# Kernel optimization log

Hardware: AMD Instinct MI355X
Metric: run time of the kernel (lower is better)

## Reference

```python
import jax, jax.numpy as jnp
import numpy as np

# CUBA LIF neuron params (from DECOLLENetwork.__init__)
THRESH = 1.25
CUR_DECAY = 0.25
VOLT_DECAY = 0.03
TAU_GRAD = 0.03
SCALE_GRAD = 3.0
SPIKE_PROB = 0.1  # input spike density


@jax.custom_vjp
def spike_fn(v):
    # Heaviside threshold with surrogate gradient (lava-dl slayer Spike)
    return (v >= THRESH).astype(v.dtype)

def _spike_fwd(v):
    return spike_fn(v), v

def _spike_bwd(v, g):
    # surrogate: scale_rho / tau_rho * exp(-|v - theta| / tau_rho)
    sg = (SCALE_GRAD / TAU_GRAD) * jnp.exp(-jnp.abs(v - THRESH) / TAU_GRAD)
    return (g * sg,)

spike_fn.defvjp(_spike_fwd, _spike_bwd)


def cuba_voltage(z):
    """Leaky-integrator recurrence over the trailing time axis.
    z: [B, N, T] synaptic current input. Returns pre-reset voltage [B, N, T].
    current[t] = (1-cd)*current[t-1] + z[t]
    voltage[t] = (1-vd)*voltage[t-1] + current[t]; hard reset to 0 on spike.
    """
    B, N, _ = z.shape
    def step(carry, zt):
        cur, volt = carry
        cur = (1.0 - CUR_DECAY) * cur + zt
        volt = (1.0 - VOLT_DECAY) * volt + cur
        volt_next = jnp.where(volt >= THRESH, 0.0, volt)  # Loihi-style hard reset
        return (cur, volt_next), volt
    init = (jnp.zeros((B, N), z.dtype), jnp.zeros((B, N), z.dtype))
    _, volts = jax.lax.scan(step, init, jnp.moveaxis(z, -1, 0))  # [T, B, N]
    return jnp.moveaxis(volts, 0, -1)  # [B, N, T]


def setup_inputs() -> dict:
    key = jax.random.key(0)
    k_x, k1, k2, k3, k4 = jax.random.split(key, 5)
    B, F_IN, T = 32, 512, 256
    H, OUT = 1024, 128
    spike = (jax.random.uniform(k_x, (B, F_IN, T)) < SPIKE_PROB).astype(jnp.float32)
    W1 = jax.random.normal(k1, (H, F_IN), jnp.float32) / np.sqrt(F_IN)
    W2 = jax.random.normal(k2, (H, H), jnp.float32) / np.sqrt(H)
    R1 = jax.random.normal(k3, (OUT, H), jnp.float32) / np.sqrt(H)
    R2 = jax.random.normal(k4, (OUT, H), jnp.float32) / np.sqrt(H)
    return {"spike": spike, "W1": W1, "W2": W2, "R1": R1, "R2": R2}


def reference(spike, W1, W2, R1, R2):
    spikes, readouts, voltages, counts = [], [], [], []
    x = spike
    for W in (W1, W2):
        # synapse: dense GEMM per timestep (input detached, DECOLLE local learning)
        z = jnp.einsum('hf,bft->bht', W, jax.lax.stop_gradient(x))
        v = cuba_voltage(z)
        s = spike_fn(v)
        voltages.append(v)
        spikes.append(s)
        counts.append(jnp.mean(jax.lax.stop_gradient(s)))
        x = s
    for R, s in zip((R1, R2), spikes):
        # readout: one batched GEMM over all timesteps (same math as per-t Linear)
        readouts.append(jnp.einsum('oh,bht->bot', R, s))
    return (tuple(spikes), tuple(readouts), tuple(voltages), tuple(counts))
```

## Files before the change

kernel.cpp:

```cpp
#include <hip/hip_runtime.h>
#include <hip/hip_bf16.h>


#define S_SZ 8388608
#define R_SZ 1048576

typedef __attribute__((ext_vector_type(8))) short v8s;
typedef __attribute__((ext_vector_type(4))) float v4f;
typedef __attribute__((ext_vector_type(8))) unsigned short u8us;

static __device__ __forceinline__ unsigned short f2bf(float x) {
  union { __hip_bfloat16 b; unsigned short u; } cv;
  cv.b = __float2bfloat16(x);
  return cv.u;
}
static __device__ __forceinline__ float bf2f(unsigned short u) {
  union { __hip_bfloat16 b; unsigned short u; } cv;
  cv.u = u;
  return __bfloat162float(cv.b);
}


__global__ __launch_bounds__(256) void split_all_kernel(
    const float* __restrict__ W1, const float* __restrict__ W2,
    const float* __restrict__ R1, const float* __restrict__ R2,
    unsigned short* __restrict__ w1s, unsigned short* __restrict__ w2s,
    unsigned short* __restrict__ r1s, unsigned short* __restrict__ r2s,
    int* __restrict__ cnt) {
  if (blockIdx.y == 0 && blockIdx.x == 0 && threadIdx.x == 0) {
    cnt[0] = 0; cnt[1] = 0;
  }
  const int i = blockIdx.x * 256 + threadIdx.x;
  const float* W; unsigned short* out; int N;
  switch (blockIdx.y) {
    case 0: W = W1; out = w1s; N = 524288; break;
    case 1: W = W2; out = w2s; N = 1048576; break;
    case 2: W = R1; out = r1s; N = 131072; break;
    default: W = R2; out = r2s; N = 131072; break;
  }
  if (i >= N) return;
  const float w0 = W[i];
  const unsigned short h = f2bf(w0);
  const float hf = bf2f(h);
  const float rm = w0 - hf;
  const unsigned short m = f2bf(rm);
  const float mf = bf2f(m);
  const unsigned short l = f2bf(rm - mf);
  out[i] = h; out[N + i] = m; out[2 * N + i] = l;
}

__global__ __launch_bounds__(256) void tcvt_kernel(const float* __restrict__ in,
                                                   unsigned short* __restrict__ out,
                                                   int R) {
  __shared__ float Ls[64][68];
  const int r0 = blockIdx.x * 64, c0 = blockIdx.y * 64, b = blockIdx.z;
  const int tid = threadIdx.x;
  const float* ip = in + ((size_t)b * R + r0) * 256 + c0;
#pragma unroll
  for (int it = 0; it < 4; ++it) {
    const int row = it * 16 + (tid >> 4), col = (tid & 15) * 4;
    const float4 v = *(const float4*)&ip[(size_t)row * 256 + col];
    *(float4*)&Ls[row][col] = v;
  }
  __syncthreads();
  const int c = tid >> 2, rs = (tid & 3) * 16;
  unsigned short h[16];
#pragma unroll
  for (int j = 0; j < 16; ++j) h[j] = f2bf(Ls[rs + j][c]);
  u8us p0, p1;
#pragma unroll
  for (int j = 0; j < 8; ++j) { p0[j] = h[j]; p1[j] = h[8 + j]; }
  unsigned short* op = out + ((size_t)b * 256 + c0 + c) * R + r0 + rs;
  *(u8us*)(op) = p0;
  *(u8us*)(op + 8) = p1;
}

__global__ __launch_bounds__(256) void gemm_mfma(
    const unsigned short* __restrict__ Asp,
    const unsigned short* __restrict__ XT,
    float* __restrict__ Z,
    int M, int K) {
  __shared__ unsigned short Alds[3 * 128 * 64];
  const int t0 = blockIdx.x * 64;
  const int m0 = blockIdx.y * 128;
  const int bg = blockIdx.z;
  const int tid = threadIdx.x;
  const int w = tid >> 6, lane = tid & 63;
  const int r = lane & 15, q = lane >> 4;
  const int wm = w >> 1, wt = w & 1;
  const int srow = lane >> 3, sslot = lane & 7;

  v4f acc[2][4][2];
#pragma unroll
  for (int ib = 0; ib < 2; ++ib)
#pragma unroll
    for (int f = 0; f < 4; ++f)
#pragma unroll
      for (int g = 0; g < 2; ++g) acc[ib][f][g] = (v4f){0.f, 0.f, 0.f, 0.f};

  const size_t MK = (size_t)M * K;
  const int nkc = K >> 6;

  for (int kc = 0; kc < nkc; ++kc) {
    const int k0 = kc << 6;
#pragma unroll
    for (int s = 0; s < 3; ++s)
#pragma unroll
      for (int c = 0; c < 4; ++c) {
        const int row = w * 32 + c * 8 + srow;
        const unsigned short* src = Asp + (size_t)s * MK + (size_t)(m0 + row) * K +
                                    k0 + ((sslot ^ (row & 7)) << 3);
        unsigned short* dst = &Alds[s * 8192 + (w * 32 + c * 8) * 64];
        __builtin_amdgcn_global_load_lds(
            (const __attribute__((address_space(1))) unsigned int*)src,
            (__attribute__((address_space(3))) unsigned int*)dst, 16, 0, 0);
      }
    v8s bfr[2][2][2];
#pragma unroll
    for (int ib = 0; ib < 2; ++ib) {
      const size_t xbase = ((size_t)(bg * 2 + ib) * 256) * K;
#pragma unroll
      for (int ks = 0; ks < 2; ++ks)
#pragma unroll
        for (int g = 0; g < 2; ++g) {
          const int t = t0 + wt * 32 + g * 16 + r;
          bfr[ib][ks][g] =
              *(const v8s*)(XT + xbase + (size_t)t * K + k0 + ks * 32 + q * 8);
        }
    }
    __syncthreads();
#pragma unroll
    for (int ks = 0; ks < 2; ++ks)
#pragma unroll
      for (int s = 0; s < 3; ++s)
#pragma unroll
        for (int f = 0; f < 4; ++f) {
          const int arow = wm * 64 + f * 16 + r;
          const v8s a = *(const v8s*)&Alds[s * 8192 + arow * 64 +
                                           (((ks * 4 + q) ^ (arow & 7)) << 3)];
#pragma unroll
          for (int ib = 0; ib < 2; ++ib) {
            acc[ib][f][0] = __builtin_amdgcn_mfma_f32_16x16x32_bf16(
                a, bfr[ib][ks][0], acc[ib][f][0], 0, 0, 0);
            acc[ib][f][1] = __builtin_amdgcn_mfma_f32_16x16x32_bf16(
                a, bfr[ib][ks][1], acc[ib][f][1], 0, 0, 0);
          }
        }
    __syncthreads();
  }
#pragma unroll
  for (int ib = 0; ib < 2; ++ib) {
    float* Zb = Z + ((size_t)(bg * 2 + ib) * M) * 256;
#pragma unroll
    for (int f = 0; f < 4; ++f)
#pragma unroll
      for (int g = 0; g < 2; ++g)
#pragma unroll
        for (int e = 0; e < 4; ++e)
          Zb[(size_t)(m0 + wm * 64 + f * 16 + q * 4 + e) * 256 +
             t0 + wt * 32 + g * 16 + r] = acc[ib][f][g][e];
  }
}

__global__ __launch_bounds__(256) void readout_mfma(
    const unsigned short* __restrict__ r1s, const unsigned short* __restrict__ r2s,
    const unsigned short* __restrict__ s1T, const unsigned short* __restrict__ s2T,
    float* __restrict__ O1, float* __restrict__ O2,
    const int* __restrict__ cnt, float* __restrict__ cc) {
  if (blockIdx.x == 0 && blockIdx.y == 0 && blockIdx.z == 0 && threadIdx.x == 0) {
    cc[0] = (float)cnt[0] * (1.0f / 8388608.0f);
    cc[1] = (float)cnt[1] * (1.0f / 8388608.0f);
  }
  const int K = 1024;
  const int t0 = blockIdx.x * 64;
  const int net = blockIdx.y;
  const int b = blockIdx.z;
  const unsigned short* __restrict__ Asp = net ? r2s : r1s;
  const unsigned short* __restrict__ XT =
      (net ? s2T : s1T) + (size_t)b * 256 * K;
  float* __restrict__ Zb = (net ? O2 : O1) + (size_t)b * 128 * 256;

  __shared__ unsigned short Alds[3 * 128 * 64];
  const int tid = threadIdx.x;
  const int w = tid >> 6, lane = tid & 63;
  const int r = lane & 15, q = lane >> 4;
  const int wm = w >> 1, wt = w & 1;
  const int srow = lane >> 3, sslot = lane & 7;

  v4f acc[4][2];
#pragma unroll
  for (int f = 0; f < 4; ++f)
#pragma unroll
    for (int g = 0; g < 2; ++g) acc[f][g] = (v4f){0.f, 0.f, 0.f, 0.f};

  const size_t MK = (size_t)128 * K;

  for (int kc = 0; kc < 16; ++kc) {
    const int k0 = kc << 6;
#pragma unroll
    for (int s = 0; s < 3; ++s)
#pragma unroll
      for (int c = 0; c < 4; ++c) {
        const int row = w * 32 + c * 8 + srow;
        const unsigned short* src = Asp + (size_t)s * MK + (size_t)row * K +
                                    k0 + ((sslot ^ (row & 7)) << 3);
        unsigned short* dst = &Alds[s * 8192 + (w * 32 + c * 8) * 64];
        __builtin_amdgcn_global_load_lds(
            (const __attribute__((address_space(1))) unsigned int*)src,
            (__attribute__((address_space(3))) unsigned int*)dst, 16, 0, 0);
      }
    v8s bfr[2][2];
#pragma unroll
    for (int ks = 0; ks < 2; ++ks)
#pragma unroll
      for (int g = 0; g < 2; ++g) {
        const int t = t0 + wt * 32 + g * 16 + r;
        bfr[ks][g] = *(const v8s*)(XT + (size_t)t * K + k0 + ks * 32 + q * 8);
      }
    __syncthreads();
#pragma unroll
    for (int ks = 0; ks < 2; ++ks)
#pragma unroll
      for (int s = 0; s < 3; ++s)
#pragma unroll
        for (int f = 0; f < 4; ++f) {
          const int arow = wm * 64 + f * 16 + r;
          const v8s a = *(const v8s*)&Alds[s * 8192 + arow * 64 +
                                           (((ks * 4 + q) ^ (arow & 7)) << 3)];
          acc[f][0] = __builtin_amdgcn_mfma_f32_16x16x32_bf16(
              a, bfr[ks][0], acc[f][0], 0, 0, 0);
          acc[f][1] = __builtin_amdgcn_mfma_f32_16x16x32_bf16(
              a, bfr[ks][1], acc[f][1], 0, 0, 0);
        }
    __syncthreads();
  }
#pragma unroll
  for (int f = 0; f < 4; ++f)
#pragma unroll
    for (int g = 0; g < 2; ++g)
#pragma unroll
      for (int e = 0; e < 4; ++e)
        Zb[(size_t)(wm * 64 + f * 16 + q * 4 + e) * 256 +
           t0 + wt * 32 + g * 16 + r] = acc[f][g][e];
}

__global__ __launch_bounds__(64) void scan_kernel(float* __restrict__ VZ,
                                                  float* __restrict__ S,
                                                  unsigned short* __restrict__ ST,
                                                  int* __restrict__ cnt) {
  const int g = blockIdx.x * 64 + threadIdx.x;
  float* vz = VZ + (size_t)g * 256;
  float* sp = S + (size_t)g * 256;
  unsigned short* st =
      ST ? ST + ((size_t)(g >> 10) * 256) * 1024 + (g & 1023) : nullptr;
  const float CD = 0.75f;
  const float VD = (float)(1.0 - 0.03);

  float4 buf[4][4];
#pragma unroll
  for (int i = 0; i < 4; ++i)
#pragma unroll
    for (int qq = 0; qq < 4; ++qq)
      buf[i][qq] = *(const float4*)(vz + i * 16 + qq * 4);

  float cur = 0.f, volt = 0.f;
  int c = 0;
#pragma unroll
  for (int tc = 0; tc < 16; ++tc) {
    float zv[16];
    *(float4*)&zv[0]  = buf[tc & 3][0];
    *(float4*)&zv[4]  = buf[tc & 3][1];
    *(float4*)&zv[8]  = buf[tc & 3][2];
    *(float4*)&zv[12] = buf[tc & 3][3];
    if (tc < 12) {
#pragma unroll
      for (int qq = 0; qq < 4; ++qq)
        buf[tc & 3][qq] = *(const float4*)(vz + (tc + 4) * 16 + qq * 4);
    }
    float vv[16], sv[16];
    unsigned short sb[16];
#pragma unroll
    for (int j = 0; j < 16; ++j) {
      cur = CD * cur + zv[j];
      volt = VD * volt + cur;
      vv[j] = volt;
      const bool spk = volt >= 1.25f;
      sv[j] = spk ? 1.0f : 0.0f;
      sb[j] = spk ? 0x3F80 : 0;
      c += spk ? 1 : 0;
      volt = spk ? 0.f : volt;
    }
    float4 o;
    o = {vv[0], vv[1], vv[2], vv[3]};     *(float4*)(vz + tc * 16 + 0) = o;
    o = {vv[4], vv[5], vv[6], vv[7]};     *(float4*)(vz + tc * 16 + 4) = o;
    o = {vv[8], vv[9], vv[10], vv[11]};   *(float4*)(vz + tc * 16 + 8) = o;
    o = {vv[12], vv[13], vv[14], vv[15]}; *(float4*)(vz + tc * 16 + 12) = o;
    o = {sv[0], sv[1], sv[2], sv[3]};     *(float4*)(sp + tc * 16 + 0) = o;
    o = {sv[4], sv[5], sv[6], sv[7]};     *(float4*)(sp + tc * 16 + 4) = o;
    o = {sv[8], sv[9], sv[10], sv[11]};   *(float4*)(sp + tc * 16 + 8) = o;
    o = {sv[12], sv[13], sv[14], sv[15]}; *(float4*)(sp + tc * 16 + 12) = o;
    if (st) {
#pragma unroll
      for (int j = 0; j < 16; ++j)
        st[(size_t)(tc * 16 + j) * 1024] = sb[j];
    }
  }
#pragma unroll
  for (int off = 32; off > 0; off >>= 1) c += __shfl_down(c, off);
  if (threadIdx.x == 0) atomicAdd(cnt, c);
}

__global__ void finalize_kernel(const int* __restrict__ cnt, float* __restrict__ c) {
  if (threadIdx.x == 0) {
    c[0] = (float)cnt[0] * (1.0f / 8388608.0f);
    c[1] = (float)cnt[1] * (1.0f / 8388608.0f);
  }
}


__global__ __launch_bounds__(256) void zero_r_kernel(float* __restrict__ r,
                                                     int* __restrict__ cnt) {
  int i = blockIdx.x * 256 + threadIdx.x;
  float4 z{0.f, 0.f, 0.f, 0.f};
  *(float4*)&r[(size_t)i * 4] = z;
  if (i == 0) { cnt[0] = 0; cnt[1] = 0; }
}

__global__ __launch_bounds__(256) void gemm_f32(
    const float* __restrict__ W, const float* __restrict__ X,
    float* __restrict__ Z, int M, int K) {
  const int T = 256;
  const int tt0 = blockIdx.x * 64;
  const int m0 = blockIdx.y * 128;
  const int b = blockIdx.z;
  const float* __restrict__ Xb = X + (size_t)b * K * T;
  float* __restrict__ Zb = Z + (size_t)b * M * T;
  __shared__ float Ws[16][132];
  __shared__ float Xs[16][68];
  const int tid = threadIdx.x;
  const int tx = tid & 15, ty = tid >> 4;
  const int ah = tid >> 1, ac = (tid & 1) * 8;
  const int bf = tid >> 4, btq = (tid & 15) * 4;
  float acc[8][4];
#pragma unroll
  for (int i = 0; i < 8; ++i)
#pragma unroll
    for (int j = 0; j < 4; ++j) acc[i][j] = 0.f;
  const float* wp = &W[(size_t)(m0 + ah) * K + ac];
  const float* xp = &Xb[(size_t)bf * T + tt0 + btq];
  for (int k0 = 0; k0 < K; k0 += 16) {
    float4 wa0 = *(const float4*)(wp + k0);
    float4 wa1 = *(const float4*)(wp + k0 + 4);
    float4 xv = *(const float4*)(xp + (size_t)k0 * T);
    __syncthreads();
    Ws[ac + 0][ah] = wa0.x; Ws[ac + 1][ah] = wa0.y;
    Ws[ac + 2][ah] = wa0.z; Ws[ac + 3][ah] = wa0.w;
    Ws[ac + 4][ah] = wa1.x; Ws[ac + 5][ah] = wa1.y;
    Ws[ac + 6][ah] = wa1.z; Ws[ac + 7][ah] = wa1.w;
    *(float4*)&Xs[bf][btq] = xv;
    __syncthreads();
#pragma unroll
    for (int f = 0; f < 16; ++f) {
      float4 a0 = *(const float4*)&Ws[f][ty * 8];
      float4 a1 = *(const float4*)&Ws[f][ty * 8 + 4];
      float4 xr = *(const float4*)&Xs[f][tx * 4];
      float av[8] = {a0.x, a0.y, a0.z, a0.w, a1.x, a1.y, a1.z, a1.w};
      float xw[4] = {xr.x, xr.y, xr.z, xr.w};
#pragma unroll
      for (int i = 0; i < 8; ++i)
#pragma unroll
        for (int j = 0; j < 4; ++j) acc[i][j] = fmaf(av[i], xw[j], acc[i][j]);
    }
  }
#pragma unroll
  for (int i = 0; i < 8; ++i) {
    float4 o{acc[i][0], acc[i][1], acc[i][2], acc[i][3]};
    *(float4*)&Zb[(size_t)(m0 + ty * 8 + i) * T + tt0 + tx * 4] = o;
  }
}

__global__ __launch_bounds__(256) void readout_kernel(
    const float* __restrict__ R1, const float* __restrict__ R2,
    const float* __restrict__ S1, const float* __restrict__ S2,
    float* __restrict__ O1, float* __restrict__ O2) {
  const int T = 256, K = 1024;
  const int tt0 = blockIdx.x * 64;
  const int kbeg = blockIdx.y * 256;
  const int zz = blockIdx.z;
  const int b = zz & 31;
  const float* __restrict__ R = (zz < 32) ? R1 : R2;
  const float* __restrict__ Sb = ((zz < 32) ? S1 : S2) + (size_t)b * K * T;
  float* __restrict__ Ob = ((zz < 32) ? O1 : O2) + (size_t)b * 128 * T;
  __shared__ float Ws[16][132];
  __shared__ float Xs[16][68];
  const int tid = threadIdx.x;
  const int tx = tid & 15, ty = tid >> 4;
  const int ah = tid >> 1, ac = (tid & 1) * 8;
  const int bf = tid >> 4, btq = (tid & 15) * 4;
  float acc[8][4];
#pragma unroll
  for (int i = 0; i < 8; ++i)
#pragma unroll
    for (int j = 0; j < 4; ++j) acc[i][j] = 0.f;
  const float* wp = &R[(size_t)ah * K + ac];
  const float* xp = &Sb[(size_t)bf * T + tt0 + btq];
  for (int k0 = kbeg; k0 < kbeg + 256; k0 += 16) {
    float4 wa0 = *(const float4*)(wp + k0);
    float4 wa1 = *(const float4*)(wp + k0 + 4);
    float4 xv = *(const float4*)(xp + (size_t)k0 * T);
    __syncthreads();
    Ws[ac + 0][ah] = wa0.x; Ws[ac + 1][ah] = wa0.y;
    Ws[ac + 2][ah] = wa0.z; Ws[ac + 3][ah] = wa0.w;
    Ws[ac + 4][ah] = wa1.x; Ws[ac + 5][ah] = wa1.y;
    Ws[ac + 6][ah] = wa1.z; Ws[ac + 7][ah] = wa1.w;
    *(float4*)&Xs[bf][btq] = xv;
    __syncthreads();
#pragma unroll
    for (int f = 0; f < 16; ++f) {
      float4 a0 = *(const float4*)&Ws[f][ty * 8];
      float4 a1 = *(const float4*)&Ws[f][ty * 8 + 4];
      float4 xr = *(const float4*)&Xs[f][tx * 4];
      float av[8] = {a0.x, a0.y, a0.z, a0.w, a1.x, a1.y, a1.z, a1.w};
      float xw[4] = {xr.x, xr.y, xr.z, xr.w};
#pragma unroll
      for (int i = 0; i < 8; ++i)
#pragma unroll
        for (int j = 0; j < 4; ++j) acc[i][j] = fmaf(av[i], xw[j], acc[i][j]);
    }
  }
#pragma unroll
  for (int i = 0; i < 8; ++i)
#pragma unroll
    for (int j = 0; j < 4; ++j)
      atomicAdd(&Ob[(size_t)(ty * 8 + i) * T + tt0 + tx * 4 + j], acc[i][j]);
}

extern "C" void kernel_launch(void* const* d_in, const int* in_sizes, int n_in,
                              void* d_out, int out_size, void* d_ws, size_t ws_size,
                              hipStream_t stream) {
  const float* spike = (const float*)d_in[0];
  const float* W1 = (const float*)d_in[1];
  const float* W2 = (const float*)d_in[2];
  const float* R1 = (const float*)d_in[3];
  const float* R2 = (const float*)d_in[4];

  float* out = (float*)d_out;
  float* s1 = out;
  float* s2 = out + S_SZ;
  float* r1 = out + 2 * S_SZ;
  float* r2 = out + 2 * S_SZ + R_SZ;
  float* v1 = out + 2 * S_SZ + 2 * R_SZ;
  float* v2 = out + 2 * S_SZ + 2 * R_SZ + S_SZ;
  float* cc = out + 4 * S_SZ + 2 * R_SZ;

  int* cnt = (int*)d_ws;
  unsigned short* w1s = (unsigned short*)((char*)d_ws + 64);
  unsigned short* w2s = w1s + 3 * 524288;
  unsigned short* r1s = w2s + 3 * 1048576;
  unsigned short* r2s = r1s + 3 * 131072;
  unsigned short* xT  = r2s + 3 * 131072;
  unsigned short* s1T = xT + 4194304;
  unsigned short* s2T = s1T + 8388608;
  const size_t WS_NEED = 53000000;

  if (ws_size >= WS_NEED) {
    split_all_kernel<<<dim3(4096, 4), 256, 0, stream>>>(W1, W2, R1, R2, w1s, w2s,
                                                        r1s, r2s, cnt);
    tcvt_kernel<<<dim3(8, 4, 32), 256, 0, stream>>>(spike, xT, 512);
    gemm_mfma<<<dim3(4, 8, 16), 256, 0, stream>>>(w1s, xT, v1, 1024, 512);
    scan_kernel<<<512, 64, 0, stream>>>(v1, s1, s1T, cnt + 0);
    gemm_mfma<<<dim3(4, 8, 16), 256, 0, stream>>>(w2s, s1T, v2, 1024, 1024);
    scan_kernel<<<512, 64, 0, stream>>>(v2, s2, s2T, cnt + 1);
    readout_mfma<<<dim3(4, 2, 32), 256, 0, stream>>>(r1s, r2s, s1T, s2T, r1, r2,
                                                     cnt, cc);
  } else {
    zero_r_kernel<<<2048, 256, 0, stream>>>(r1, cnt);
    gemm_f32<<<dim3(4, 8, 32), 256, 0, stream>>>(W1, spike, v1, 1024, 512);
    scan_kernel<<<512, 64, 0, stream>>>(v1, s1, nullptr, cnt + 0);
    gemm_f32<<<dim3(4, 8, 32), 256, 0, stream>>>(W2, s1, v2, 1024, 1024);
    scan_kernel<<<512, 64, 0, stream>>>(v2, s2, nullptr, cnt + 1);
    readout_kernel<<<dim3(4, 4, 64), 256, 0, stream>>>(R1, R2, s1, s2, r1, r2);
    finalize_kernel<<<1, 1, 0, stream>>>(cnt, cc);
  }
}
```

Baseline: 347.9 us.

## Double-buffer split-A LDS tiles to overlap global loads with MFMA compute

Both the layer GEMM and readout GEMM now keep two LDS buffers, each holding one bf16 split slice of the A tile. The next slice is prefetched while MFMAs run on the current one, and B fragments are loaded ahead in alternating register sets. Previously all three slices were loaded, then a barrier, then compute, with no overlap. The cost is three times as many barriers per K-chunk and extra registers for two B fragment sets, which may lower occupancy.

```diff
diff --git a/kernel.cpp b/kernel.cpp
--- a/kernel.cpp
+++ b/kernel.cpp
@@ -80,7 +80,7 @@
     const unsigned short* __restrict__ XT,
     float* __restrict__ Z,
     int M, int K) {
-  __shared__ unsigned short Alds[3 * 128 * 64];
+  __shared__ unsigned short Alds[2][128 * 64];
   const int t0 = blockIdx.x * 64;
   const int m0 = blockIdx.y * 128;
   const int bg = blockIdx.z;
@@ -89,33 +89,32 @@
   const int r = lane & 15, q = lane >> 4;
   const int wm = w >> 1, wt = w & 1;
   const int srow = lane >> 3, sslot = lane & 7;
-
-  v4f acc[2][4][2];
-#pragma unroll
-  for (int ib = 0; ib < 2; ++ib)
-#pragma unroll
-    for (int f = 0; f < 4; ++f)
-#pragma unroll
-      for (int g = 0; g < 2; ++g) acc[ib][f][g] = (v4f){0.f, 0.f, 0.f, 0.f};
-
   const size_t MK = (size_t)M * K;
   const int nkc = K >> 6;
 
-  for (int kc = 0; kc < nkc; ++kc) {
+  v4f acc[2][4][2];
+#pragma unroll
+  for (int ib = 0; ib < 2; ++ib)
+#pragma unroll
+    for (int f = 0; f < 4; ++f)
+#pragma unroll
+      for (int g = 0; g < 2; ++g) acc[ib][f][g] = (v4f){0.f, 0.f, 0.f, 0.f};
+
+  auto STAGE = [&](int buf, int s, int kc) {
     const int k0 = kc << 6;
 #pragma unroll
-    for (int s = 0; s < 3; ++s)
-#pragma unroll
-      for (int c = 0; c < 4; ++c) {
-        const int row = w * 32 + c * 8 + srow;
-        const unsigned short* src = Asp + (size_t)s * MK + (size_t)(m0 + row) * K +
-                                    k0 + ((sslot ^ (row & 7)) << 3);
-        unsigned short* dst = &Alds[s * 8192 + (w * 32 + c * 8) * 64];
-        __builtin_amdgcn_global_load_lds(
-            (const __attribute__((address_space(1))) unsigned int*)src,
-            (__attribute__((address_space(3))) unsigned int*)dst, 16, 0, 0);
-      }
-    v8s bfr[2][2][2];
+    for (int c = 0; c < 4; ++c) {
+      const int row = w * 32 + c * 8 + srow;
+      const unsigned short* src = Asp + (size_t)s * MK + (size_t)(m0 + row) * K +
+                                  k0 + ((sslot ^ (row & 7)) << 3);
+      unsigned short* dst = &Alds[buf][(w * 32 + c * 8) * 64];
+      __builtin_amdgcn_global_load_lds(
+          (const __attribute__((address_space(1))) unsigned int*)src,
+          (__attribute__((address_space(3))) unsigned int*)dst, 16, 0, 0);
+    }
+  };
+  auto BLOAD = [&](v8s (&bfr)[2][2][2], int kc) {
+    const int k0 = kc << 6;
 #pragma unroll
     for (int ib = 0; ib < 2; ++ib) {
       const size_t xbase = ((size_t)(bg * 2 + ib) * 256) * K;
@@ -128,26 +127,41 @@
               *(const v8s*)(XT + xbase + (size_t)t * K + k0 + ks * 32 + q * 8);
         }
     }
-    __syncthreads();
+  };
+  auto COMPUTE = [&](int buf, v8s (&bfr)[2][2][2]) {
 #pragma unroll
     for (int ks = 0; ks < 2; ++ks)
 #pragma unroll
-      for (int s = 0; s < 3; ++s)
-#pragma unroll
-        for (int f = 0; f < 4; ++f) {
-          const int arow = wm * 64 + f * 16 + r;
-          const v8s a = *(const v8s*)&Alds[s * 8192 + arow * 64 +
+      for (int f = 0; f < 4; ++f) {
+        const int arow = wm * 64 + f * 16 + r;
+        const v8s a = *(const v8s*)&Alds[buf][arow * 64 +
                                            (((ks * 4 + q) ^ (arow & 7)) << 3)];
 #pragma unroll
-          for (int ib = 0; ib < 2; ++ib) {
-            acc[ib][f][0] = __builtin_amdgcn_mfma_f32_16x16x32_bf16(
-                a, bfr[ib][ks][0], acc[ib][f][0], 0, 0, 0);
-            acc[ib][f][1] = __builtin_amdgcn_mfma_f32_16x16x32_bf16(
-                a, bfr[ib][ks][1], acc[ib][f][1], 0, 0, 0);
-          }
+        for (int ib = 0; ib < 2; ++ib) {
+          acc[ib][f][0] = __builtin_amdgcn_mfma_f32_16x16x32_bf16(
+              a, bfr[ib][ks][0], acc[ib][f][0], 0, 0, 0);
+          acc[ib][f][1] = __builtin_amdgcn_mfma_f32_16x16x32_bf16(
+              a, bfr[ib][ks][1], acc[ib][f][1], 0, 0, 0);
         }
-    __syncthreads();
-  }
+      }
+  };
+
+  v8s bA[2][2][2], bB[2][2][2];
+  STAGE(0, 0, 0);
+  BLOAD(bA, 0);
+  __syncthreads();
+  int buf = 0;
+  for (int kc = 0; kc < nkc; kc += 2) {
+    STAGE(buf ^ 1, 1, kc);     COMPUTE(buf, bA); __syncthreads(); buf ^= 1;
+    STAGE(buf ^ 1, 2, kc);     COMPUTE(buf, bA); __syncthreads(); buf ^= 1;
+    STAGE(buf ^ 1, 0, kc + 1); BLOAD(bB, kc + 1);
+                               COMPUTE(buf, bA); __syncthreads(); buf ^= 1;
+    STAGE(buf ^ 1, 1, kc + 1); COMPUTE(buf, bB); __syncthreads(); buf ^= 1;
+    STAGE(buf ^ 1, 2, kc + 1); COMPUTE(buf, bB); __syncthreads(); buf ^= 1;
+    if (kc + 2 < nkc) { STAGE(buf ^ 1, 0, kc + 2); BLOAD(bA, kc + 2); }
+                               COMPUTE(buf, bB); __syncthreads(); buf ^= 1;
+  }
+
 #pragma unroll
   for (int ib = 0; ib < 2; ++ib) {
     float* Zb = Z + ((size_t)(bg * 2 + ib) * M) * 256;
@@ -176,16 +190,17 @@
   const int net = blockIdx.y;
   const int b = blockIdx.z;
   const unsigned short* __restrict__ Asp = net ? r2s : r1s;
-  const unsigned short* __restrict__ XT =
-      (net ? s2T : s1T) + (size_t)b * 256 * K;
+  const unsigned short* __restrict__ XT = (net ? s2T : s1T) + (size_t)b * 256 * K;
   float* __restrict__ Zb = (net ? O2 : O1) + (size_t)b * 128 * 256;
 
-  __shared__ unsigned short Alds[3 * 128 * 64];
+  __shared__ unsigned short Alds[2][128 * 64];
   const int tid = threadIdx.x;
   const int w = tid >> 6, lane = tid & 63;
   const int r = lane & 15, q = lane >> 4;
   const int wm = w >> 1, wt = w & 1;
   const int srow = lane >> 3, sslot = lane & 7;
+  const size_t MK = (size_t)128 * K;
+  const int nkc = 16;
 
   v4f acc[4][2];
 #pragma unroll
@@ -193,23 +208,21 @@
 #pragma unroll
     for (int g = 0; g < 2; ++g) acc[f][g] = (v4f){0.f, 0.f, 0.f, 0.f};
 
-  const size_t MK = (size_t)128 * K;
-
-  for (int kc = 0; kc < 16; ++kc) {
+  auto STAGE = [&](int buf, int s, int kc) {
     const int k0 = kc << 6;
 #pragma unroll
-    for (int s = 0; s < 3; ++s)
-#pragma unroll
-      for (int c = 0; c < 4; ++c) {
-        const int row = w * 32 + c * 8 + srow;
-        const unsigned short* src = Asp + (size_t)s * MK + (size_t)row * K +
-                                    k0 + ((sslot ^ (row & 7)) << 3);
-        unsigned short* dst = &Alds[s * 8192 + (w * 32 + c * 8) * 64];
-        __builtin_amdgcn_global_load_lds(
-            (const __attribute__((address_space(1))) unsigned int*)src,
-            (__attribute__((address_space(3))) unsigned int*)dst, 16, 0, 0);
-      }
-    v8s bfr[2][2];
+    for (int c = 0; c < 4; ++c) {
+      const int row = w * 32 + c * 8 + srow;
+      const unsigned short* src = Asp + (size_t)s * MK + (size_t)row * K +
+                                  k0 + ((sslot ^ (row & 7)) << 3);
+      unsigned short* dst = &Alds[buf][(w * 32 + c * 8) * 64];
+      __builtin_amdgcn_global_load_lds(
+          (const __attribute__((address_space(1))) unsigned int*)src,
+          (__attribute__((address_space(3))) unsigned int*)dst, 16, 0, 0);
+    }
+  };
+  auto BLOAD = [&](v8s (&bfr)[2][2], int kc) {
+    const int k0 = kc << 6;
 #pragma unroll
     for (int ks = 0; ks < 2; ++ks)
 #pragma unroll
@@ -217,23 +230,38 @@
         const int t = t0 + wt * 32 + g * 16 + r;
         bfr[ks][g] = *(const v8s*)(XT + (size_t)t * K + k0 + ks * 32 + q * 8);
       }
-    __syncthreads();
+  };
+  auto COMPUTE = [&](int buf, v8s (&bfr)[2][2]) {
 #pragma unroll
     for (int ks = 0; ks < 2; ++ks)
 #pragma unroll
-      for (int s = 0; s < 3; ++s)
-#pragma unroll
-        for (int f = 0; f < 4; ++f) {
-          const int arow = wm * 64 + f * 16 + r;
-          const v8s a = *(const v8s*)&Alds[s * 8192 + arow * 64 +
+      for (int f = 0; f < 4; ++f) {
+        const int arow = wm * 64 + f * 16 + r;
+        const v8s a = *(const v8s*)&Alds[buf][arow * 64 +
                                            (((ks * 4 + q) ^ (arow & 7)) << 3)];
-          acc[f][0] = __builtin_amdgcn_mfma_f32_16x16x32_bf16(
-              a, bfr[ks][0], acc[f][0], 0, 0, 0);
-          acc[f][1] = __builtin_amdgcn_mfma_f32_16x16x32_bf16(
-              a, bfr[ks][1], acc[f][1], 0, 0, 0);
-        }
-    __syncthreads();
-  }
+        acc[f][0] = __builtin_amdgcn_mfma_f32_16x16x32_bf16(
+            a, bfr[ks][0], acc[f][0], 0, 0, 0);
+        acc[f][1] = __builtin_amdgcn_mfma_f32_16x16x32_bf16(
+            a, bfr[ks][1], acc[f][1], 0, 0, 0);
+      }
+  };
+
+  v8s bA[2][2], bB[2][2];
+  STAGE(0, 0, 0);
+  BLOAD(bA, 0);
+  __syncthreads();
+  int buf = 0;
+  for (int kc = 0; kc < nkc; kc += 2) {
+    STAGE(buf ^ 1, 1, kc);     COMPUTE(buf, bA); __syncthreads(); buf ^= 1;
+    STAGE(buf ^ 1, 2, kc);     COMPUTE(buf, bA); __syncthreads(); buf ^= 1;
+    STAGE(buf ^ 1, 0, kc + 1); BLOAD(bB, kc + 1);
+                               COMPUTE(buf, bA); __syncthreads(); buf ^= 1;
+    STAGE(buf ^ 1, 1, kc + 1); COMPUTE(buf, bB); __syncthreads(); buf ^= 1;
+    STAGE(buf ^ 1, 2, kc + 1); COMPUTE(buf, bB); __syncthreads(); buf ^= 1;
+    if (kc + 2 < nkc) { STAGE(buf ^ 1, 0, kc + 2); BLOAD(bA, kc + 2); }
+                               COMPUTE(buf, bB); __syncthreads(); buf ^= 1;
+  }
+
 #pragma unroll
   for (int f = 0; f < 4; ++f)
 #pragma unroll
```

Result: no change. 346.1 us (-0.5%).

## Use two-term bf16 weight split and load GEMM operands directly to registers

Applied to the files above, without the earlier changes.

Weights are now split into two bf16 terms instead of three, which cuts MFMA work and weight traffic by a third. The GEMM and readout kernels no longer stage A tiles through LDS with global_load_lds and barriers. Each wave instead loads its A and B fragments straight from global memory into registers. This removes the synchronisation and LDS traffic, but A rows are now reloaded per wave without sharing, and the two-term split lowers weight precision, which may matter near the spike threshold.

```diff
diff --git a/kernel.cpp b/kernel.cpp
--- a/kernel.cpp
+++ b/kernel.cpp
@@ -42,11 +42,8 @@
   const float w0 = W[i];
   const unsigned short h = f2bf(w0);
   const float hf = bf2f(h);
-  const float rm = w0 - hf;
-  const unsigned short m = f2bf(rm);
-  const float mf = bf2f(m);
-  const unsigned short l = f2bf(rm - mf);
-  out[i] = h; out[N + i] = m; out[2 * N + i] = l;
+  const unsigned short m = f2bf(w0 - hf);
+  out[i] = h; out[N + i] = m;
 }
 
 __global__ __launch_bounds__(256) void tcvt_kernel(const float* __restrict__ in,
@@ -75,12 +72,11 @@
   *(u8us*)(op + 8) = p1;
 }
 
-__global__ __launch_bounds__(256) void gemm_mfma(
+__global__ __launch_bounds__(256) void gemm_mfma_reg(
     const unsigned short* __restrict__ Asp,
     const unsigned short* __restrict__ XT,
     float* __restrict__ Z,
     int M, int K) {
-  __shared__ unsigned short Alds[3 * 128 * 64];
   const int t0 = blockIdx.x * 64;
   const int m0 = blockIdx.y * 128;
   const int bg = blockIdx.z;
@@ -88,66 +84,57 @@
   const int w = tid >> 6, lane = tid & 63;
   const int r = lane & 15, q = lane >> 4;
   const int wm = w >> 1, wt = w & 1;
-  const int srow = lane >> 3, sslot = lane & 7;
-
-  v4f acc[2][4][2];
-#pragma unroll
-  for (int ib = 0; ib < 2; ++ib)
-#pragma unroll
-    for (int f = 0; f < 4; ++f)
-#pragma unroll
-      for (int g = 0; g < 2; ++g) acc[ib][f][g] = (v4f){0.f, 0.f, 0.f, 0.f};
-
   const size_t MK = (size_t)M * K;
   const int nkc = K >> 6;
 
+  v4f acc[2][4][2];
+#pragma unroll
+  for (int ib = 0; ib < 2; ++ib)
+#pragma unroll
+    for (int f = 0; f < 4; ++f)
+#pragma unroll
+      for (int g = 0; g < 2; ++g) acc[ib][f][g] = (v4f){0.f, 0.f, 0.f, 0.f};
+
+  const unsigned short* aB = Asp + (size_t)(m0 + wm * 64 + r) * K + q * 8;
+  const unsigned short* bB0 =
+      XT + ((size_t)(bg * 2 + 0) * 256 + t0 + wt * 32 + r) * K + q * 8;
+  const unsigned short* bB1 =
+      XT + ((size_t)(bg * 2 + 1) * 256 + t0 + wt * 32 + r) * K + q * 8;
+
   for (int kc = 0; kc < nkc; ++kc) {
     const int k0 = kc << 6;
-#pragma unroll
-    for (int s = 0; s < 3; ++s)
-#pragma unroll
-      for (int c = 0; c < 4; ++c) {
-        const int row = w * 32 + c * 8 + srow;
-        const unsigned short* src = Asp + (size_t)s * MK + (size_t)(m0 + row) * K +
-                                    k0 + ((sslot ^ (row & 7)) << 3);
-        unsigned short* dst = &Alds[s * 8192 + (w * 32 + c * 8) * 64];
-        __builtin_amdgcn_global_load_lds(
-            (const __attribute__((address_space(1))) unsigned int*)src,
-            (__attribute__((address_space(3))) unsigned int*)dst, 16, 0, 0);
+    v8s b[2][2][2];
+#pragma unroll
+    for (int ks = 0; ks < 2; ++ks)
+#pragma unroll
+      for (int g = 0; g < 2; ++g) {
+        b[0][ks][g] = *(const v8s*)(bB0 + (size_t)(g * 16) * K + k0 + ks * 32);
+        b[1][ks][g] = *(const v8s*)(bB1 + (size_t)(g * 16) * K + k0 + ks * 32);
       }
-    v8s bfr[2][2][2];
-#pragma unroll
-    for (int ib = 0; ib < 2; ++ib) {
-      const size_t xbase = ((size_t)(bg * 2 + ib) * 256) * K;
+    v8s a[2][4][2];
+#pragma unroll
+    for (int s = 0; s < 2; ++s)
+#pragma unroll
+      for (int f = 0; f < 4; ++f)
+#pragma unroll
+        for (int ks = 0; ks < 2; ++ks)
+          a[s][f][ks] =
+              *(const v8s*)(aB + s * MK + (size_t)(f * 16) * K + k0 + ks * 32);
+#pragma unroll
+    for (int s = 0; s < 2; ++s)
 #pragma unroll
       for (int ks = 0; ks < 2; ++ks)
 #pragma unroll
-        for (int g = 0; g < 2; ++g) {
-          const int t = t0 + wt * 32 + g * 16 + r;
-          bfr[ib][ks][g] =
-              *(const v8s*)(XT + xbase + (size_t)t * K + k0 + ks * 32 + q * 8);
-        }
-    }
-    __syncthreads();
-#pragma unroll
-    for (int ks = 0; ks < 2; ++ks)
-#pragma unroll
-      for (int s = 0; s < 3; ++s)
-#pragma unroll
-        for (int f = 0; f < 4; ++f) {
-          const int arow = wm * 64 + f * 16 + r;
-          const v8s a = *(const v8s*)&Alds[s * 8192 + arow * 64 +
-                                           (((ks * 4 + q) ^ (arow & 7)) << 3)];
+        for (int f = 0; f < 4; ++f)
 #pragma unroll
           for (int ib = 0; ib < 2; ++ib) {
             acc[ib][f][0] = __builtin_amdgcn_mfma_f32_16x16x32_bf16(
-                a, bfr[ib][ks][0], acc[ib][f][0], 0, 0, 0);
+                a[s][f][ks], b[ib][ks][0], acc[ib][f][0], 0, 0, 0);
             acc[ib][f][1] = __builtin_amdgcn_mfma_f32_16x16x32_bf16(
-                a, bfr[ib][ks][1], acc[ib][f][1], 0, 0, 0);
+                a[s][f][ks], b[ib][ks][1], acc[ib][f][1], 0, 0, 0);
           }
-        }
-    __syncthreads();
-  }
+  }
+
 #pragma unroll
   for (int ib = 0; ib < 2; ++ib) {
     float* Zb = Z + ((size_t)(bg * 2 + ib) * M) * 256;
@@ -162,7 +149,7 @@
   }
 }
 
-__global__ __launch_bounds__(256) void readout_mfma(
+__global__ __launch_bounds__(256) void readout_mfma_reg(
     const unsigned short* __restrict__ r1s, const unsigned short* __restrict__ r2s,
     const unsigned short* __restrict__ s1T, const unsigned short* __restrict__ s2T,
     float* __restrict__ O1, float* __restrict__ O2,
@@ -176,16 +163,14 @@
   const int net = blockIdx.y;
   const int b = blockIdx.z;
   const unsigned short* __restrict__ Asp = net ? r2s : r1s;
-  const unsigned short* __restrict__ XT =
-      (net ? s2T : s1T) + (size_t)b * 256 * K;
+  const unsigned short* __restrict__ XT = (net ? s2T : s1T) + (size_t)b * 256 * K;
   float* __restrict__ Zb = (net ? O2 : O1) + (size_t)b * 128 * 256;
 
-  __shared__ unsigned short Alds[3 * 128 * 64];
   const int tid = threadIdx.x;
   const int w = tid >> 6, lane = tid & 63;
   const int r = lane & 15, q = lane >> 4;
   const int wm = w >> 1, wt = w & 1;
-  const int srow = lane >> 3, sslot = lane & 7;
+  const size_t MK = (size_t)128 * K;
 
   v4f acc[4][2];
 #pragma unroll
@@ -193,47 +178,39 @@
 #pragma unroll
     for (int g = 0; g < 2; ++g) acc[f][g] = (v4f){0.f, 0.f, 0.f, 0.f};
 
-  const size_t MK = (size_t)128 * K;
+  const unsigned short* aB = Asp + (size_t)(wm * 64 + r) * K + q * 8;
+  const unsigned short* bB = XT + (size_t)(t0 + wt * 32 + r) * K + q * 8;
 
   for (int kc = 0; kc < 16; ++kc) {
     const int k0 = kc << 6;
-#pragma unroll
-    for (int s = 0; s < 3; ++s)
-#pragma unroll
-      for (int c = 0; c < 4; ++c) {
-        const int row = w * 32 + c * 8 + srow;
-        const unsigned short* src = Asp + (size_t)s * MK + (size_t)row * K +
-                                    k0 + ((sslot ^ (row & 7)) << 3);
-        unsigned short* dst = &Alds[s * 8192 + (w * 32 + c * 8) * 64];
-        __builtin_amdgcn_global_load_lds(
-            (const __attribute__((address_space(1))) unsigned int*)src,
-            (__attribute__((address_space(3))) unsigned int*)dst, 16, 0, 0);
-      }
-    v8s bfr[2][2];
+    v8s b[2][2];
 #pragma unroll
     for (int ks = 0; ks < 2; ++ks)
 #pragma unroll
-      for (int g = 0; g < 2; ++g) {
-        const int t = t0 + wt * 32 + g * 16 + r;
-        bfr[ks][g] = *(const v8s*)(XT + (size_t)t * K + k0 + ks * 32 + q * 8);
-      }
-    __syncthreads();
-#pragma unroll
-    for (int ks = 0; ks < 2; ++ks)
-#pragma unroll
-      for (int s = 0; s < 3; ++s)
+      for (int g = 0; g < 2; ++g)
+        b[ks][g] = *(const v8s*)(bB + (size_t)(g * 16) * K + k0 + ks * 32);
+    v8s a[2][4][2];
+#pragma unroll
+    for (int s = 0; s < 2; ++s)
+#pragma unroll
+      for (int f = 0; f < 4; ++f)
+#pragma unroll
+        for (int ks = 0; ks < 2; ++ks)
+          a[s][f][ks] =
+              *(const v8s*)(aB + s * MK + (size_t)(f * 16) * K + k0 + ks * 32);
+#pragma unroll
+    for (int s = 0; s < 2; ++s)
+#pragma unroll
+      for (int ks = 0; ks < 2; ++ks)
 #pragma unroll
         for (int f = 0; f < 4; ++f) {
-          const int arow = wm * 64 + f * 16 + r;
-          const v8s a = *(const v8s*)&Alds[s * 8192 + arow * 64 +
-                                           (((ks * 4 + q) ^ (arow & 7)) << 3)];
           acc[f][0] = __builtin_amdgcn_mfma_f32_16x16x32_bf16(
-              a, bfr[ks][0], acc[f][0], 0, 0, 0);
+              a[s][f][ks], b[ks][0], acc[f][0], 0, 0, 0);
           acc[f][1] = __builtin_amdgcn_mfma_f32_16x16x32_bf16(
-              a, bfr[ks][1], acc[f][1], 0, 0, 0);
+              a[s][f][ks], b[ks][1], acc[f][1], 0, 0, 0);
         }
-    __syncthreads();
-  }
+  }
+
 #pragma unroll
   for (int f = 0; f < 4; ++f)
 #pragma unroll
@@ -455,24 +432,24 @@
 
   int* cnt = (int*)d_ws;
   unsigned short* w1s = (unsigned short*)((char*)d_ws + 64);
-  unsigned short* w2s = w1s + 3 * 524288;
-  unsigned short* r1s = w2s + 3 * 1048576;
-  unsigned short* r2s = r1s + 3 * 131072;
-  unsigned short* xT  = r2s + 3 * 131072;
+  unsigned short* w2s = w1s + 2 * 524288;
+  unsigned short* r1s = w2s + 2 * 1048576;
+  unsigned short* r2s = r1s + 2 * 131072;
+  unsigned short* xT  = r2s + 2 * 131072;
   unsigned short* s1T = xT + 4194304;
   unsigned short* s2T = s1T + 8388608;
-  const size_t WS_NEED = 53000000;
+  const size_t WS_NEED = 48000000;
 
   if (ws_size >= WS_NEED) {
     split_all_kernel<<<dim3(4096, 4), 256, 0, stream>>>(W1, W2, R1, R2, w1s, w2s,
                                                         r1s, r2s, cnt);
     tcvt_kernel<<<dim3(8, 4, 32), 256, 0, stream>>>(spike, xT, 512);
-    gemm_mfma<<<dim3(4, 8, 16), 256, 0, stream>>>(w1s, xT, v1, 1024, 512);
+    gemm_mfma_reg<<<dim3(4, 8, 16), 256, 0, stream>>>(w1s, xT, v1, 1024, 512);
     scan_kernel<<<512, 64, 0, stream>>>(v1, s1, s1T, cnt + 0);
-    gemm_mfma<<<dim3(4, 8, 16), 256, 0, stream>>>(w2s, s1T, v2, 1024, 1024);
+    gemm_mfma_reg<<<dim3(4, 8, 16), 256, 0, stream>>>(w2s, s1T, v2, 1024, 1024);
     scan_kernel<<<512, 64, 0, stream>>>(v2, s2, s2T, cnt + 1);
-    readout_mfma<<<dim3(4, 2, 32), 256, 0, stream>>>(r1s, r2s, s1T, s2T, r1, r2,
-                                                     cnt, cc);
+    readout_mfma_reg<<<dim3(4, 2, 32), 256, 0, stream>>>(r1s, r2s, s1T, s2T, r1,
+                                                         r2, cnt, cc);
   } else {
     zero_r_kernel<<<2048, 256, 0, stream>>>(r1, cnt);
     gemm_f32<<<dim3(4, 8, 32), 256, 0, stream>>>(W1, spike, v1, 1024, 512);
```

Measured after the change: 398.8 us. 1.15x slower.
